# Kernel tuning notes

Hardware: AMD Instinct MI355X
Metric: run time of the kernel (lower is better)

Reference implementation:

```python
import jax, jax.numpy as jnp
import numpy as np

N_NODES = 50000
N_EDGES = 800000
IN_C = 128
HID = 128
OUT_C = 64
N_GRAPHS = 256


def setup_inputs() -> dict:
    key = jax.random.key(0)
    ks = jax.random.split(key, 12)
    x = jax.random.normal(ks[0], (N_NODES, IN_C), dtype=jnp.float32)
    edge_index = jax.random.randint(ks[1], (2, N_EDGES), 0, N_NODES, dtype=jnp.int32)
    batch = jnp.sort(jax.random.randint(ks[2], (N_NODES,), 0, N_GRAPHS, dtype=jnp.int32))
    def lin(k, fan_in, fan_out):
        bound = 1.0 / np.sqrt(fan_in)
        kw, kb = jax.random.split(k)
        W = jax.random.uniform(kw, (fan_in, fan_out), minval=-bound, maxval=bound, dtype=jnp.float32)
        b = jax.random.uniform(kb, (fan_out,), minval=-bound, maxval=bound, dtype=jnp.float32)
        return W, b
    W1a, b1a = lin(ks[3], IN_C, HID)
    W1b, b1b = lin(ks[4], HID, HID)
    W2a, b2a = lin(ks[5], HID, HID)
    W2b, b2b = lin(ks[6], HID, HID)
    Wl, bl = lin(ks[7], HID, OUT_C)
    return {"x": x, "edge_index": edge_index, "batch": batch,
            "W1a": W1a, "b1a": b1a, "W1b": W1b, "b1b": b1b,
            "W2a": W2a, "b2a": b2a, "W2b": W2b, "b2b": b2b,
            "Wl": Wl, "bl": bl}


def gin_conv(x, edge_index, Wa, ba, Wb, bb):
    # GINConv with eps=0: h_i = MLP(x_i + sum_{j->i} x_j)
    src, dst = edge_index[0], edge_index[1]
    agg = jax.ops.segment_sum(x[src], dst, num_segments=x.shape[0])  # [N, d]
    h = x + agg
    h = jax.nn.relu(h @ Wa + ba) @ Wb + bb
    return h


def reference(x, edge_index, batch, W1a, b1a, W1b, b1b, W2a, b2a, W2b, b2b, Wl, bl):
    h = gin_conv(x, edge_index, W1a, b1a, W1b, b1b)
    h = gin_conv(h, edge_index, W2a, b2a, W2b, b2b)
    # global mean pool over graphs in the batch
    sums = jax.ops.segment_sum(h, batch, num_segments=N_GRAPHS)          # [G, HID]
    cnts = jax.ops.segment_sum(jnp.ones((h.shape[0],), h.dtype), batch, num_segments=N_GRAPHS)
    pooled = sums / jnp.maximum(cnts, 1.0)[:, None]
    return pooled @ Wl + bl  # [G, OUT_C]
```

## Files before the change

### kernel.cpp

```cpp
#include <hip/hip_runtime.h>

constexpr int N  = 50000;
constexpr int E  = 800000;
constexpr int C  = 128;
constexpr int G  = 256;
constexpr int OC = 64;
constexpr int D  = 64;

constexpr int NBUCK = 196;
constexpr int BCAP  = 5120;
constexpr int EB = (E + 4095) / 4096;
constexpr int WB = 256;
constexpr int XB = (N * C / 8 + 255) / 256;

typedef __attribute__((ext_vector_type(8))) short short8;
typedef __attribute__((ext_vector_type(4))) float f32x4;
typedef __attribute__((ext_vector_type(2))) float f32x2;

__device__ __forceinline__ unsigned int au(float f) { return __float_as_uint(f); }

__device__ __forceinline__ unsigned short f2bf(float f) {
    unsigned int u = au(f);
    u += 0x7fffu + ((u >> 16) & 1u);
    return (unsigned short)(u >> 16);
}
__device__ __forceinline__ unsigned int pack_bf16(float lo, float hi) {
    return ((au(hi) + 0x8000u) & 0xFFFF0000u) | ((au(lo) + 0x8000u) >> 16);
}

__device__ __forceinline__ void acc16(f32x2* a, uint4 v) {
    a[0] += __builtin_amdgcn_cvt_pk_f32_fp8((int)v.x, false);
    a[1] += __builtin_amdgcn_cvt_pk_f32_fp8((int)v.x, true);
    a[2] += __builtin_amdgcn_cvt_pk_f32_fp8((int)v.y, false);
    a[3] += __builtin_amdgcn_cvt_pk_f32_fp8((int)v.y, true);
    a[4] += __builtin_amdgcn_cvt_pk_f32_fp8((int)v.z, false);
    a[5] += __builtin_amdgcn_cvt_pk_f32_fp8((int)v.z, true);
    a[6] += __builtin_amdgcn_cvt_pk_f32_fp8((int)v.w, false);
    a[7] += __builtin_amdgcn_cvt_pk_f32_fp8((int)v.w, true);
}
__device__ __forceinline__ void set16(f32x2* a, uint4 v) {
    a[0] = __builtin_amdgcn_cvt_pk_f32_fp8((int)v.x, false);
    a[1] = __builtin_amdgcn_cvt_pk_f32_fp8((int)v.x, true);
    a[2] = __builtin_amdgcn_cvt_pk_f32_fp8((int)v.y, false);
    a[3] = __builtin_amdgcn_cvt_pk_f32_fp8((int)v.y, true);
    a[4] = __builtin_amdgcn_cvt_pk_f32_fp8((int)v.z, false);
    a[5] = __builtin_amdgcn_cvt_pk_f32_fp8((int)v.z, true);
    a[6] = __builtin_amdgcn_cvt_pk_f32_fp8((int)v.w, false);
    a[7] = __builtin_amdgcn_cvt_pk_f32_fp8((int)v.w, true);
}


__global__ __launch_bounds__(256) void build_prep_kernel(const int* __restrict__ src,
                                                         const int* __restrict__ dst,
                                                         int* __restrict__ bcount,
                                                         unsigned int* __restrict__ bucketbuf,
                                                         const float* __restrict__ W1a,
                                                         const float* __restrict__ W1b,
                                                         const float* __restrict__ W2a,
                                                         const float* __restrict__ W2b,
                                                         const float* __restrict__ x,
                                                         unsigned short* __restrict__ wt,
                                                         unsigned int* __restrict__ x8) {
    int b = blockIdx.x;
    if (b < EB) {
        __shared__ int lcount[NBUCK];
        __shared__ int lbase[NBUCK];
        __shared__ int lcur[NBUCK];
        int tid = threadIdx.x;
        for (int i = tid; i < NBUCK; i += 256) { lcount[i] = 0; lcur[i] = 0; }
        __syncthreads();
        int e0 = b * 4096;
        int sv[16], dv[16];
#pragma unroll
        for (int i = 0; i < 16; ++i) {
            int e = e0 + i * 256 + tid;
            if (e < E) {
                sv[i] = src[e];
                dv[i] = dst[e];
                atomicAdd(&lcount[dv[i] >> 8], 1);
            } else {
                dv[i] = -1;
            }
        }
        __syncthreads();
        if (tid < NBUCK) {
            int c = lcount[tid];
            lbase[tid] = (c > 0) ? atomicAdd(&bcount[tid], c) : 0;
        }
        __syncthreads();
#pragma unroll
        for (int i = 0; i < 16; ++i) {
            if (dv[i] >= 0) {
                int bk = dv[i] >> 8;
                int pos = lbase[bk] + atomicAdd(&lcur[bk], 1);
                if (pos < BCAP)
                    bucketbuf[(size_t)bk * BCAP + pos] =
                        ((unsigned int)sv[i] << 16) | (unsigned int)(dv[i] & 255);
            }
        }
    } else if (b < EB + WB) {
        const float* Ws[4] = {W1a, W1b, W2a, W2b};
        int idx = (b - EB) * 256 + threadIdx.x;
        int which = idx >> 14;
        int el    = idx & 16383;
        int n = el >> 7, k = el & 127;
        wt[idx] = f2bf(Ws[which][k * 128 + n]);
    } else {
        int idx = (b - EB - WB) * 256 + threadIdx.x;
        const float4* x4 = (const float4*)x;
        float4 v0 = x4[idx * 2];
        float4 v1 = x4[idx * 2 + 1];
        unsigned int lo = 0, hi = 0;
        lo = (unsigned int)__builtin_amdgcn_cvt_pk_fp8_f32(v0.x, v0.y, (int)lo, false);
        lo = (unsigned int)__builtin_amdgcn_cvt_pk_fp8_f32(v0.z, v0.w, (int)lo, true);
        hi = (unsigned int)__builtin_amdgcn_cvt_pk_fp8_f32(v1.x, v1.y, (int)hi, false);
        hi = (unsigned int)__builtin_amdgcn_cvt_pk_fp8_f32(v1.z, v1.w, (int)hi, true);
        ((uint2*)x8)[idx] = make_uint2(lo, hi);
    }
}


__global__ __launch_bounds__(256) void bucket_fill_kernel(const int* __restrict__ bcount,
                                                          const unsigned int* __restrict__ bucketbuf,
                                                          unsigned short* __restrict__ ell,
                                                          int* __restrict__ deg) {
    __shared__ int lcur[256];
    int b = blockIdx.x;
    int tid = threadIdx.x;
    lcur[tid] = 0;
    __syncthreads();
    int cnt = min(bcount[b], BCAP);
    const unsigned int* buf = bucketbuf + (size_t)b * BCAP;
    int nbase = b << 8;
    for (int i = tid; i < cnt; i += 256) {
        unsigned int e = buf[i];
        int dlow = (int)(e & 255u);
        int s = (int)(e >> 16);
        int p = atomicAdd(&lcur[dlow], 1);
        if (p < D) ell[(size_t)p * N + nbase + dlow] = (unsigned short)s;
    }
    __syncthreads();
    int node = nbase + tid;
    if (node < N) deg[node] = lcur[tid];
}


__global__ __launch_bounds__(256) void aggregate_kernel(const unsigned char* __restrict__ Fg,
                                                        const int* __restrict__ deg,
                                                        const unsigned short* __restrict__ ell,
                                                        unsigned short* __restrict__ Y) {
    int grp = threadIdx.x >> 3;
    int l   = threadIdx.x & 7;
    int n = blockIdx.x * 32 + grp;
    if (n >= N) return;
    const uint4* F16 = (const uint4*)Fg;
    f32x2 a[8];
    int dg = min(deg[n], D);
    const unsigned short* ecol = ell + n;
    set16(a, F16[(size_t)n * 8 + l]);
    int j = 0;
    if (dg >= 8) {
        int i0 = ecol[0];
        int i1 = ecol[(size_t)1 * N];
        int i2 = ecol[(size_t)2 * N];
        int i3 = ecol[(size_t)3 * N];
        int i4 = ecol[(size_t)4 * N];
        int i5 = ecol[(size_t)5 * N];
        int i6 = ecol[(size_t)6 * N];
        int i7 = ecol[(size_t)7 * N];
        uint4 v0 = F16[(size_t)i0 * 8 + l];
        uint4 v1 = F16[(size_t)i1 * 8 + l];
        uint4 v2 = F16[(size_t)i2 * 8 + l];
        uint4 v3 = F16[(size_t)i3 * 8 + l];
        uint4 v4 = F16[(size_t)i4 * 8 + l];
        uint4 v5 = F16[(size_t)i5 * 8 + l];
        uint4 v6 = F16[(size_t)i6 * 8 + l];
        uint4 v7 = F16[(size_t)i7 * 8 + l];
        for (j = 8; j + 8 <= dg; j += 8) {
            int t0 = ecol[(size_t)(j + 0) * N];
            int t1 = ecol[(size_t)(j + 1) * N];
            int t2 = ecol[(size_t)(j + 2) * N];
            int t3 = ecol[(size_t)(j + 3) * N];
            int t4 = ecol[(size_t)(j + 4) * N];
            int t5 = ecol[(size_t)(j + 5) * N];
            int t6 = ecol[(size_t)(j + 6) * N];
            int t7 = ecol[(size_t)(j + 7) * N];
            uint4 w0 = F16[(size_t)t0 * 8 + l];
            uint4 w1 = F16[(size_t)t1 * 8 + l];
            uint4 w2 = F16[(size_t)t2 * 8 + l];
            uint4 w3 = F16[(size_t)t3 * 8 + l];
            uint4 w4 = F16[(size_t)t4 * 8 + l];
            uint4 w5 = F16[(size_t)t5 * 8 + l];
            uint4 w6 = F16[(size_t)t6 * 8 + l];
            uint4 w7 = F16[(size_t)t7 * 8 + l];
            acc16(a, v0); acc16(a, v1); acc16(a, v2); acc16(a, v3);
            acc16(a, v4); acc16(a, v5); acc16(a, v6); acc16(a, v7);
            v0 = w0; v1 = w1; v2 = w2; v3 = w3;
            v4 = w4; v5 = w5; v6 = w6; v7 = w7;
        }
        acc16(a, v0); acc16(a, v1); acc16(a, v2); acc16(a, v3);
        acc16(a, v4); acc16(a, v5); acc16(a, v6); acc16(a, v7);
    }
    for (; j < dg; ++j) {
        uint4 v = F16[(size_t)ecol[(size_t)j * N] * 8 + l];
        acc16(a, v);
    }
    uint4 o0, o1;
    o0.x = pack_bf16(a[0].x, a[0].y); o0.y = pack_bf16(a[1].x, a[1].y);
    o0.z = pack_bf16(a[2].x, a[2].y); o0.w = pack_bf16(a[3].x, a[3].y);
    o1.x = pack_bf16(a[4].x, a[4].y); o1.y = pack_bf16(a[5].x, a[5].y);
    o1.z = pack_bf16(a[6].x, a[6].y); o1.w = pack_bf16(a[7].x, a[7].y);
    uint4* yp = (uint4*)(Y + (size_t)n * 128 + l * 16);
    yp[0] = o0;
    yp[1] = o1;
}


__global__ __launch_bounds__(256) void mlp_kernel(const unsigned short* __restrict__ Xg,
                                                  const unsigned short* __restrict__ WaT,
                                                  const float* __restrict__ ba,
                                                  const unsigned short* __restrict__ WbT,
                                                  const float* __restrict__ bb,
                                                  unsigned char* __restrict__ Hg8,
                                                  unsigned short* __restrict__ Hgb,
                                                  int outFp8) {
    constexpr int LD = 136;
    __shared__ short Xl[64 * LD];
    __shared__ short Wl[128 * LD];
    int tid  = threadIdx.x;
    int lane = tid & 63;
    int wave = tid >> 6;
    int row0 = blockIdx.x * 64;

    const short8* Xg8 = (const short8*)(Xg + (size_t)row0 * 128);
#pragma unroll
    for (int i = tid; i < 1024; i += 256) {
        int r = i >> 4, c = i & 15;
        *((short8*)(Xl + r * LD) + c) = Xg8[i];
    }
    const short8* Wa8 = (const short8*)WaT;
#pragma unroll
    for (int i = tid; i < 2048; i += 256) {
        int r = i >> 4, c = i & 15;
        *((short8*)(Wl + r * LD) + c) = Wa8[i];
    }

    int mw = wave >> 1, nw = wave & 1;
    int lid = lane & 15, quad = lane >> 4;

    f32x4 acc[2][4];
#pragma unroll
    for (int nt = 0; nt < 4; ++nt) {
        float b = ba[nw * 64 + nt * 16 + lid];
        acc[0][nt] = (f32x4){b, b, b, b};
        acc[1][nt] = (f32x4){b, b, b, b};
    }
    __syncthreads();

#pragma unroll
    for (int ks = 0; ks < 4; ++ks) {
        short8 a0 = *(const short8*)(Xl + (mw * 32 + lid) * LD + ks * 32 + quad * 8);
        short8 a1 = *(const short8*)(Xl + (mw * 32 + 16 + lid) * LD + ks * 32 + quad * 8);
#pragma unroll
        for (int nt = 0; nt < 4; ++nt) {
            short8 bf = *(const short8*)(Wl + (nw * 64 + nt * 16 + lid) * LD + ks * 32 + quad * 8);
            acc[0][nt] = __builtin_amdgcn_mfma_f32_16x16x32_bf16(a0, bf, acc[0][nt], 0, 0, 0);
            acc[1][nt] = __builtin_amdgcn_mfma_f32_16x16x32_bf16(a1, bf, acc[1][nt], 0, 0, 0);
        }
    }
    __syncthreads();

#pragma unroll
    for (int mt = 0; mt < 2; ++mt) {
#pragma unroll
        for (int nt = 0; nt < 4; ++nt) {
            int mbase = mw * 32 + mt * 16 + quad * 4;
            int n = nw * 64 + nt * 16 + lid;
            f32x4 v = acc[mt][nt];
#pragma unroll
            for (int r = 0; r < 4; ++r)
                Xl[(mbase + r) * LD + n] = (short)f2bf(fmaxf(v[r], 0.f));
        }
    }
    const short8* Wb8 = (const short8*)WbT;
#pragma unroll
    for (int i = tid; i < 2048; i += 256) {
        int r = i >> 4, c = i & 15;
        *((short8*)(Wl + r * LD) + c) = Wb8[i];
    }
    f32x4 acc2[2][4];
#pragma unroll
    for (int nt = 0; nt < 4; ++nt) {
        float b = bb[nw * 64 + nt * 16 + lid];
        acc2[0][nt] = (f32x4){b, b, b, b};
        acc2[1][nt] = (f32x4){b, b, b, b};
    }
    __syncthreads();

#pragma unroll
    for (int ks = 0; ks < 4; ++ks) {
        short8 a0 = *(const short8*)(Xl + (mw * 32 + lid) * LD + ks * 32 + quad * 8);
        short8 a1 = *(const short8*)(Xl + (mw * 32 + 16 + lid) * LD + ks * 32 + quad * 8);
#pragma unroll
        for (int nt = 0; nt < 4; ++nt) {
            short8 bf = *(const short8*)(Wl + (nw * 64 + nt * 16 + lid) * LD + ks * 32 + quad * 8);
            acc2[0][nt] = __builtin_amdgcn_mfma_f32_16x16x32_bf16(a0, bf, acc2[0][nt], 0, 0, 0);
            acc2[1][nt] = __builtin_amdgcn_mfma_f32_16x16x32_bf16(a1, bf, acc2[1][nt], 0, 0, 0);
        }
    }

#pragma unroll
    for (int mt = 0; mt < 2; ++mt) {
#pragma unroll
        for (int nt = 0; nt < 4; ++nt) {
            int mbase = row0 + mw * 32 + mt * 16 + quad * 4;
            int n = nw * 64 + nt * 16 + lid;
            f32x4 v = acc2[mt][nt];
            if (outFp8) {
#pragma unroll
                for (int r = 0; r < 4; ++r) {
                    int row = mbase + r;
                    if (row < N) {
                        unsigned int p = (unsigned int)__builtin_amdgcn_cvt_pk_fp8_f32(v[r], 0.f, 0, false);
                        Hg8[(size_t)row * 128 + n] = (unsigned char)(p & 0xFF);
                    }
                }
            } else {
#pragma unroll
                for (int r = 0; r < 4; ++r) {
                    int row = mbase + r;
                    if (row < N) Hgb[(size_t)row * 128 + n] = f2bf(v[r]);
                }
            }
        }
    }
}


__global__ __launch_bounds__(256) void pool_partial_kernel(const unsigned short* __restrict__ H,
                                                           const int* __restrict__ batch,
                                                           float* __restrict__ gsum,
                                                           int* __restrict__ gcnt) {
    int tid = threadIdx.x;
    int w = tid >> 6;
    int l = tid & 63;
    int r0 = blockIdx.x * 64 + w * 16;
    if (r0 >= N) return;
    int rend = min(r0 + 16, N);
    const unsigned int* H2 = (const unsigned int*)H;
    int curg = batch[r0];
    int runstart = r0;
    float a0 = 0.f, a1 = 0.f;
    for (int r = r0; r < rend; ++r) {
        int g = batch[r];
        if (g != curg) {
            atomicAdd(&gsum[curg * C + 2 * l], a0);
            atomicAdd(&gsum[curg * C + 2 * l + 1], a1);
            if (l == 0) atomicAdd(&gcnt[curg], r - runstart);
            curg = g; runstart = r; a0 = 0.f; a1 = 0.f;
        }
        unsigned int v = H2[(size_t)r * 64 + l];
        a0 += __uint_as_float((v & 0xffffu) << 16);
        a1 += __uint_as_float(v & 0xffff0000u);
    }
    atomicAdd(&gsum[curg * C + 2 * l], a0);
    atomicAdd(&gsum[curg * C + 2 * l + 1], a1);
    if (l == 0) atomicAdd(&gcnt[curg], rend - runstart);
}


__global__ __launch_bounds__(64) void head_kernel(const float* __restrict__ gsum,
                                                  const int* __restrict__ gcnt,
                                                  const float* __restrict__ Wl,
                                                  const float* __restrict__ bl,
                                                  float* __restrict__ out) {
    int g = blockIdx.x;
    int t = threadIdx.x;
    __shared__ float pooled[C];
    float inv = 1.0f / (float)max(gcnt[g], 1);
    pooled[t]      = gsum[g * C + t] * inv;
    pooled[t + 64] = gsum[g * C + 64 + t] * inv;
    __syncthreads();
    float o = bl[t];
#pragma unroll 4
    for (int k = 0; k < C; ++k) o += pooled[k] * Wl[k * OC + t];
    out[g * OC + t] = o;
}


extern "C" void kernel_launch(void* const* d_in, const int* in_sizes, int n_in,
                              void* d_out, int out_size, void* d_ws, size_t ws_size,
                              hipStream_t stream) {
    const float* x    = (const float*)d_in[0];
    const int*   ei   = (const int*)d_in[1];
    const int*   bat  = (const int*)d_in[2];
    const float* W1a  = (const float*)d_in[3];
    const float* b1a  = (const float*)d_in[4];
    const float* W1b  = (const float*)d_in[5];
    const float* b1b  = (const float*)d_in[6];
    const float* W2a  = (const float*)d_in[7];
    const float* b2a  = (const float*)d_in[8];
    const float* W2b  = (const float*)d_in[9];
    const float* b2b  = (const float*)d_in[10];
    const float* Wl   = (const float*)d_in[11];
    const float* bl   = (const float*)d_in[12];
    float*       out  = (float*)d_out;

    float* gsum    = (float*)d_ws;
    int*   gcnt    = (int*)(gsum + G * C);
    int*   bcount  = gcnt + G;
    int*   deg     = bcount + NBUCK;
    unsigned int* bucketbuf = (unsigned int*)(deg + N);
    unsigned short* ell = (unsigned short*)(bucketbuf + (size_t)NBUCK * BCAP);
    unsigned short* wt  = ell + (size_t)N * D;
    unsigned char*  x8  = (unsigned char*)(wt + 4 * 16384);
    unsigned char*  h8  = x8 + (size_t)N * 128;
    unsigned short* y   = (unsigned short*)(h8 + (size_t)N * 128);
    unsigned short* hb  = y + (size_t)(N + 64) * 128;

    const unsigned short* wt1a = wt;
    const unsigned short* wt1b = wt + 16384;
    const unsigned short* wt2a = wt + 2 * 16384;
    const unsigned short* wt2b = wt + 3 * 16384;

    const int* src = ei;
    const int* dst = ei + E;

    hipMemsetAsync(gsum, 0, (size_t)(G * C + G + NBUCK) * sizeof(int), stream);

    build_prep_kernel<<<EB + WB + XB, 256, 0, stream>>>(src, dst, bcount, bucketbuf,
                                                        W1a, W1b, W2a, W2b, x,
                                                        wt, (unsigned int*)x8);
    bucket_fill_kernel<<<NBUCK, 256, 0, stream>>>(bcount, bucketbuf, ell, deg);

    int ab = (N + 31) / 32;
    int mb = (N + 63) / 64;

    aggregate_kernel<<<ab, 256, 0, stream>>>(x8, deg, ell, y);
    mlp_kernel<<<mb, 256, 0, stream>>>(y, wt1a, b1a, wt1b, b1b, h8, nullptr, 1);

    aggregate_kernel<<<ab, 256, 0, stream>>>(h8, deg, ell, y);
    mlp_kernel<<<mb, 256, 0, stream>>>(y, wt2a, b2a, wt2b, b2b, nullptr, hb, 0);

    pool_partial_kernel<<<mb, 256, 0, stream>>>(hb, bat, gsum, gcnt);
    head_kernel<<<G, 64, 0, stream>>>(gsum, gcnt, Wl, bl, out);
}
```

Before: 221.2 us.

## Split fp8 feature tables into two channel planes and aggregate each separately

```diff
diff --git a/kernel.cpp b/kernel.cpp
--- a/kernel.cpp
+++ b/kernel.cpp
@@ -16,6 +16,7 @@
 typedef __attribute__((ext_vector_type(8))) short short8;
 typedef __attribute__((ext_vector_type(4))) float f32x4;
 typedef __attribute__((ext_vector_type(2))) float f32x2;
+typedef __attribute__((ext_vector_type(4))) unsigned int u32x4;
 
 __device__ __forceinline__ unsigned int au(float f) { return __float_as_uint(f); }
 
@@ -115,7 +116,9 @@
         lo = (unsigned int)__builtin_amdgcn_cvt_pk_fp8_f32(v0.z, v0.w, (int)lo, true);
         hi = (unsigned int)__builtin_amdgcn_cvt_pk_fp8_f32(v1.x, v1.y, (int)hi, false);
         hi = (unsigned int)__builtin_amdgcn_cvt_pk_fp8_f32(v1.z, v1.w, (int)hi, true);
-        ((uint2*)x8)[idx] = make_uint2(lo, hi);
+        int n = idx >> 4, c8 = idx & 15;
+        int plane = c8 >> 3;
+        ((uint2*)x8)[(size_t)plane * N * 8 + (size_t)n * 8 + (c8 & 7)] = make_uint2(lo, hi);
     }
 }
 
@@ -145,19 +148,20 @@
 }
 
 
-__global__ __launch_bounds__(256) void aggregate_kernel(const unsigned char* __restrict__ Fg,
+__global__ __launch_bounds__(256) void aggregate_kernel(const unsigned char* __restrict__ Fp,
                                                         const int* __restrict__ deg,
                                                         const unsigned short* __restrict__ ell,
-                                                        unsigned short* __restrict__ Y) {
-    int grp = threadIdx.x >> 3;
-    int l   = threadIdx.x & 7;
-    int n = blockIdx.x * 32 + grp;
+                                                        unsigned short* __restrict__ Y,
+                                                        int chanOff) {
+    int grp = threadIdx.x >> 2;
+    int l   = threadIdx.x & 3;
+    int n = blockIdx.x * 64 + grp;
     if (n >= N) return;
-    const uint4* F16 = (const uint4*)Fg;
+    const uint4* F4 = (const uint4*)Fp;
     f32x2 a[8];
     int dg = min(deg[n], D);
     const unsigned short* ecol = ell + n;
-    set16(a, F16[(size_t)n * 8 + l]);
+    set16(a, F4[(size_t)n * 4 + l]);
     int j = 0;
     if (dg >= 8) {
         int i0 = ecol[0];
@@ -168,14 +172,14 @@
         int i5 = ecol[(size_t)5 * N];
         int i6 = ecol[(size_t)6 * N];
         int i7 = ecol[(size_t)7 * N];
-        uint4 v0 = F16[(size_t)i0 * 8 + l];
-        uint4 v1 = F16[(size_t)i1 * 8 + l];
-        uint4 v2 = F16[(size_t)i2 * 8 + l];
-        uint4 v3 = F16[(size_t)i3 * 8 + l];
-        uint4 v4 = F16[(size_t)i4 * 8 + l];
-        uint4 v5 = F16[(size_t)i5 * 8 + l];
-        uint4 v6 = F16[(size_t)i6 * 8 + l];
-        uint4 v7 = F16[(size_t)i7 * 8 + l];
+        uint4 v0 = F4[(size_t)i0 * 4 + l];
+        uint4 v1 = F4[(size_t)i1 * 4 + l];
+        uint4 v2 = F4[(size_t)i2 * 4 + l];
+        uint4 v3 = F4[(size_t)i3 * 4 + l];
+        uint4 v4 = F4[(size_t)i4 * 4 + l];
+        uint4 v5 = F4[(size_t)i5 * 4 + l];
+        uint4 v6 = F4[(size_t)i6 * 4 + l];
+        uint4 v7 = F4[(size_t)i7 * 4 + l];
         for (j = 8; j + 8 <= dg; j += 8) {
             int t0 = ecol[(size_t)(j + 0) * N];
             int t1 = ecol[(size_t)(j + 1) * N];
@@ -185,14 +189,14 @@
             int t5 = ecol[(size_t)(j + 5) * N];
             int t6 = ecol[(size_t)(j + 6) * N];
             int t7 = ecol[(size_t)(j + 7) * N];
-            uint4 w0 = F16[(size_t)t0 * 8 + l];
-            uint4 w1 = F16[(size_t)t1 * 8 + l];
-            uint4 w2 = F16[(size_t)t2 * 8 + l];
-            uint4 w3 = F16[(size_t)t3 * 8 + l];
-            uint4 w4 = F16[(size_t)t4 * 8 + l];
-            uint4 w5 = F16[(size_t)t5 * 8 + l];
-            uint4 w6 = F16[(size_t)t6 * 8 + l];
-            uint4 w7 = F16[(size_t)t7 * 8 + l];
+            uint4 w0 = F4[(size_t)t0 * 4 + l];
+            uint4 w1 = F4[(size_t)t1 * 4 + l];
+            uint4 w2 = F4[(size_t)t2 * 4 + l];
+            uint4 w3 = F4[(size_t)t3 * 4 + l];
+            uint4 w4 = F4[(size_t)t4 * 4 + l];
+            uint4 w5 = F4[(size_t)t5 * 4 + l];
+            uint4 w6 = F4[(size_t)t6 * 4 + l];
+            uint4 w7 = F4[(size_t)t7 * 4 + l];
             acc16(a, v0); acc16(a, v1); acc16(a, v2); acc16(a, v3);
             acc16(a, v4); acc16(a, v5); acc16(a, v6); acc16(a, v7);
             v0 = w0; v1 = w1; v2 = w2; v3 = w3;
@@ -202,17 +206,17 @@
         acc16(a, v4); acc16(a, v5); acc16(a, v6); acc16(a, v7);
     }
     for (; j < dg; ++j) {
-        uint4 v = F16[(size_t)ecol[(size_t)j * N] * 8 + l];
+        uint4 v = F4[(size_t)ecol[(size_t)j * N] * 4 + l];
         acc16(a, v);
     }
-    uint4 o0, o1;
+    u32x4 o0, o1;
     o0.x = pack_bf16(a[0].x, a[0].y); o0.y = pack_bf16(a[1].x, a[1].y);
     o0.z = pack_bf16(a[2].x, a[2].y); o0.w = pack_bf16(a[3].x, a[3].y);
     o1.x = pack_bf16(a[4].x, a[4].y); o1.y = pack_bf16(a[5].x, a[5].y);
     o1.z = pack_bf16(a[6].x, a[6].y); o1.w = pack_bf16(a[7].x, a[7].y);
-    uint4* yp = (uint4*)(Y + (size_t)n * 128 + l * 16);
-    yp[0] = o0;
-    yp[1] = o1;
+    u32x4* yp = (u32x4*)(Y + (size_t)n * 128 + chanOff + l * 16);
+    __builtin_nontemporal_store(o0, yp);
+    __builtin_nontemporal_store(o1, yp + 1);
 }
 
 
@@ -322,7 +326,8 @@
                     int row = mbase + r;
                     if (row < N) {
                         unsigned int p = (unsigned int)__builtin_amdgcn_cvt_pk_fp8_f32(v[r], 0.f, 0, false);
-                        Hg8[(size_t)row * 128 + n] = (unsigned char)(p & 0xFF);
+                        Hg8[(size_t)nw * N * 64 + (size_t)row * 64 + nt * 16 + lid] =
+                            (unsigned char)(p & 0xFF);
                     }
                 }
             } else {
@@ -433,13 +438,15 @@
                                                         wt, (unsigned int*)x8);
     bucket_fill_kernel<<<NBUCK, 256, 0, stream>>>(bcount, bucketbuf, ell, deg);
 
-    int ab = (N + 31) / 32;
+    int ab = (N + 63) / 64;
     int mb = (N + 63) / 64;
 
-    aggregate_kernel<<<ab, 256, 0, stream>>>(x8, deg, ell, y);
+    aggregate_kernel<<<ab, 256, 0, stream>>>(x8,                  deg, ell, y, 0);
+    aggregate_kernel<<<ab, 256, 0, stream>>>(x8 + (size_t)N * 64, deg, ell, y, 64);
     mlp_kernel<<<mb, 256, 0, stream>>>(y, wt1a, b1a, wt1b, b1b, h8, nullptr, 1);
 
-    aggregate_kernel<<<ab, 256, 0, stream>>>(h8, deg, ell, y);
+    aggregate_kernel<<<ab, 256, 0, stream>>>(h8,                  deg, ell, y, 0);
+    aggregate_kernel<<<ab, 256, 0, stream>>>(h8 + (size_t)N * 64, deg, ell, y, 64);
     mlp_kernel<<<mb, 256, 0, stream>>>(y, wt2a, b2a, wt2b, b2b, nullptr, hb, 0);
 
     pool_partial_kernel<<<mb, 256, 0, stream>>>(hb, bat, gsum, gcnt);
```

Measured after the change: 231.4 us. 1.05x slower.
